# Optimization experiments

Measured on AMD Instinct MI355X. Metric: run time of the kernel, lower is better.

Reference implementation:

```python
import jax, jax.numpy as jnp
import numpy as np

N_NODES = 100000
N_EDGES = 1600000
NFEAT, NHID, NCLASS = 512, 128, 40


def setup_inputs() -> dict:
    key = jax.random.key(0)
    ks = jax.random.split(key, 8)
    x = jax.random.normal(ks[0], (N_NODES, NFEAT), dtype=jnp.float32)
    adj_row = jax.random.randint(ks[1], (N_EDGES,), 0, N_NODES, dtype=jnp.int64)
    adj_col = jax.random.randint(ks[2], (N_EDGES,), 0, N_NODES, dtype=jnp.int64)
    adj_val = jax.random.uniform(ks[3], (N_EDGES,), dtype=jnp.float32)
    W1 = jax.random.normal(ks[4], (NFEAT, NHID), dtype=jnp.float32) * (1.0 / np.sqrt(NHID))
    b1 = jax.random.normal(ks[5], (NHID,), dtype=jnp.float32) * 0.01
    W2 = jax.random.normal(ks[6], (NHID, NCLASS), dtype=jnp.float32) * (1.0 / np.sqrt(NCLASS))
    b2 = jax.random.normal(ks[7], (NCLASS,), dtype=jnp.float32) * 0.01
    return {"x": x, "adj_row": adj_row, "adj_col": adj_col, "adj_val": adj_val,
            "W1": W1, "b1": b1, "W2": W2, "b2": b2}


def _spmm(row, col, val, dense):
    # COO SpMM: out[r] = sum_e val[e] * dense[col[e]]  for edges with row[e]==r
    gathered = val[:, None] * dense[col]          # [E, F]
    return jax.ops.segment_sum(gathered, row, num_segments=N_NODES)


def reference(x, adj_row, adj_col, adj_val, W1, b1, W2, b2):
    # Layer 1: support = X @ W1; out = A @ support + b1; ReLU
    h = _spmm(adj_row, adj_col, adj_val, x @ W1) + b1
    h = jax.nn.relu(h)
    # dropout is identity in eval mode (training=False)
    # Layer 2
    logits = _spmm(adj_row, adj_col, adj_val, h @ W2) + b2
    return jax.nn.log_softmax(logits, axis=1)
```

## Files before the change

kernel.cpp:

```cpp
#include <hip/hip_runtime.h>
#include <hip/hip_bf16.h>
#include <math.h>

#define N_NODES 100000
#define N_EDGES 1600000
#define NFEAT 512
#define NHID 128
#define NCLASS 40
#define GEMM1_BLOCKS ((N_NODES + 255) / 256)
#define COUNT_BLOCKS ((N_EDGES + 255) / 256)
#define CPAD 16

typedef __attribute__((ext_vector_type(8))) short short8;
typedef __attribute__((ext_vector_type(4))) float floatx4;

__device__ __forceinline__ short f2bf(float f) {
    union { float f; unsigned u; } v; v.f = f;
    unsigned r = v.u + 0x7FFFu + ((v.u >> 16) & 1u);
    return (short)(r >> 16);
}
__device__ __forceinline__ float bf2f(unsigned short u) {
    union { unsigned u; float f; } v; v.u = ((unsigned)u) << 16;
    return v.f;
}
__device__ __forceinline__ unsigned pk2bf(float a, float b) {
    __hip_bfloat162 t = __float22bfloat162_rn(make_float2(a, b));
    union { __hip_bfloat162 h; unsigned u; } v; v.h = t;
    return v.u;
}

__global__ void convert_W1_kernel(const float* __restrict__ W1, unsigned short* __restrict__ W1T) {
    int i = blockIdx.x * 256 + threadIdx.x;
    int k = i >> 7, n = i & 127;
    W1T[(size_t)n * NFEAT + k] = (unsigned short)f2bf(W1[i]);
}

__global__ __launch_bounds__(256, 2)
void fusedA_kernel(const float* __restrict__ x, const unsigned short* __restrict__ W1T,
                   unsigned short* __restrict__ out,
                   const int* __restrict__ adj_row, int* __restrict__ countsPad) {
    if (blockIdx.x >= GEMM1_BLOCKS) {
        int e = (blockIdx.x - GEMM1_BLOCKS) * 256 + threadIdx.x;
        if (e < N_EDGES) atomicAdd(&countsPad[(size_t)adj_row[e] * CPAD], 1);
        return;
    }
    int t = threadIdx.x;
    int w = t >> 6, l = t & 63;
    int lane16 = l & 15, quad = l >> 4;
    int rowBase = blockIdx.x * 256 + w * 64;

    floatx4 acc[4][8];
    #pragma unroll
    for (int i = 0; i < 4; i++)
        #pragma unroll
        for (int j = 0; j < 8; j++) acc[i][j] = (floatx4){0.f, 0.f, 0.f, 0.f};

    for (int kc = 0; kc < NFEAT; kc += 32) {
        short8 bfr[8];
        #pragma unroll
        for (int nt = 0; nt < 8; nt++) {
            const unsigned short* bp =
                W1T + (size_t)(nt * 16 + lane16) * NFEAT + kc + quad * 8;
            bfr[nt] = *(const short8*)bp;
        }
        short8 afr[4];
        #pragma unroll
        for (int mt = 0; mt < 4; mt++) {
            int gr = rowBase + mt * 16 + lane16;
            if (gr >= N_NODES) gr = N_NODES - 1;
            const float* ap = x + (size_t)gr * NFEAT + kc + quad * 8;
            float4 v0 = *(const float4*)ap;
            float4 v1 = *(const float4*)(ap + 4);
            union { short8 s; unsigned u[4]; } av;
            av.u[0] = pk2bf(v0.x, v0.y);
            av.u[1] = pk2bf(v0.z, v0.w);
            av.u[2] = pk2bf(v1.x, v1.y);
            av.u[3] = pk2bf(v1.z, v1.w);
            afr[mt] = av.s;
        }
        #pragma unroll
        for (int mt = 0; mt < 4; mt++)
            #pragma unroll
            for (int nt = 0; nt < 8; nt++)
                acc[mt][nt] = __builtin_amdgcn_mfma_f32_16x16x32_bf16(
                    afr[mt], bfr[nt], acc[mt][nt], 0, 0, 0);
    }
    #pragma unroll
    for (int mt = 0; mt < 4; mt++) {
        #pragma unroll
        for (int r = 0; r < 4; r++) {
            int gr = rowBase + mt * 16 + quad * 4 + r;
            if (gr < N_NODES) {
                #pragma unroll
                for (int nt = 0; nt < 8; nt++)
                    out[(size_t)gr * NHID + nt * 16 + lane16] =
                        (unsigned short)f2bf(acc[mt][nt][r]);
            }
        }
    }
}

__global__ void scan1_kernel(const int* __restrict__ countsPad, int* __restrict__ offsets,
                             int* __restrict__ blockSums, int n) {
    __shared__ int sdata[256];
    int t = threadIdx.x;
    int base = blockIdx.x * 1024 + t * 4;
    int v0 = (base + 0 < n) ? countsPad[(size_t)(base + 0) * CPAD] : 0;
    int v1 = (base + 1 < n) ? countsPad[(size_t)(base + 1) * CPAD] : 0;
    int v2 = (base + 2 < n) ? countsPad[(size_t)(base + 2) * CPAD] : 0;
    int v3 = (base + 3 < n) ? countsPad[(size_t)(base + 3) * CPAD] : 0;
    int tot = v0 + v1 + v2 + v3;
    sdata[t] = tot;
    __syncthreads();
    for (int ofs = 1; ofs < 256; ofs <<= 1) {
        int w = (t >= ofs) ? sdata[t - ofs] : 0;
        __syncthreads();
        sdata[t] += w;
        __syncthreads();
    }
    int excl = sdata[t] - tot;
    if (base + 0 < n) offsets[base + 0] = excl;
    if (base + 1 < n) offsets[base + 1] = excl + v0;
    if (base + 2 < n) offsets[base + 2] = excl + v0 + v1;
    if (base + 3 < n) offsets[base + 3] = excl + v0 + v1 + v2;
    if (t == 255) blockSums[blockIdx.x] = sdata[255];
}

__global__ void scan2_kernel(int* __restrict__ blockSums, int nb) {
    __shared__ int sdata[128];
    int t = threadIdx.x;
    int v = (t < nb) ? blockSums[t] : 0;
    sdata[t] = v;
    __syncthreads();
    for (int ofs = 1; ofs < 128; ofs <<= 1) {
        int w = (t >= ofs) ? sdata[t - ofs] : 0;
        __syncthreads();
        sdata[t] += w;
        __syncthreads();
    }
    if (t < nb) blockSums[t] = sdata[t] - v;
}

__global__ void scan3_kernel(int* __restrict__ offsets, const int* __restrict__ blockSums,
                             int* __restrict__ cursorPad, int n, int total) {
    int t = threadIdx.x;
    int base = blockIdx.x * 1024 + t * 4;
    int add = blockSums[blockIdx.x];
    #pragma unroll
    for (int j = 0; j < 4; j++)
        if (base + j < n) {
            int v = offsets[base + j] + add;
            offsets[base + j] = v;
            cursorPad[(size_t)(base + j) * CPAD] = v;
        }
    if (blockIdx.x == 0 && t == 0) offsets[n] = total;
}

__global__ void fill_kernel(const int* __restrict__ row, const int* __restrict__ col,
                            const float* __restrict__ val, int* __restrict__ cursorPad,
                            int2* __restrict__ csr, int E) {
    int e = blockIdx.x * blockDim.x + threadIdx.x;
    if (e < E) {
        int r = row[e];
        int p = atomicAdd(&cursorPad[(size_t)r * CPAD], 1);
        csr[p] = make_int2(col[e], __float_as_int(val[e]));
    }
}

__global__ __launch_bounds__(256)
void spmm1_kernel(const int* __restrict__ offsets, const int2* __restrict__ csr,
                  const unsigned short* __restrict__ dense, const float* __restrict__ b1,
                  unsigned short* __restrict__ h) {
    int r = blockIdx.x * 4 + (threadIdx.x >> 6);
    int l = threadIdx.x & 63;
    int beg = offsets[r], end = offsets[r + 1];
    float acc0 = 0.f, acc1 = 0.f;
    for (int c0 = beg; c0 < end; c0 += 64) {
        int cnt = min(64, end - c0);
        int2 pk = (l < cnt) ? csr[c0 + l] : make_int2(0, 0);
        int j = 0;
        for (; j + 4 <= cnt; j += 4) {
            int cA = __shfl(pk.x, j + 0), cB = __shfl(pk.x, j + 1);
            int cC = __shfl(pk.x, j + 2), cD = __shfl(pk.x, j + 3);
            float vA = __int_as_float(__shfl(pk.y, j + 0));
            float vB = __int_as_float(__shfl(pk.y, j + 1));
            float vC = __int_as_float(__shfl(pk.y, j + 2));
            float vD = __int_as_float(__shfl(pk.y, j + 3));
            unsigned dA = *(const unsigned*)&dense[(size_t)cA * NHID + l * 2];
            unsigned dB = *(const unsigned*)&dense[(size_t)cB * NHID + l * 2];
            unsigned dC = *(const unsigned*)&dense[(size_t)cC * NHID + l * 2];
            unsigned dD = *(const unsigned*)&dense[(size_t)cD * NHID + l * 2];
            acc0 += vA * bf2f((unsigned short)dA) + vB * bf2f((unsigned short)dB)
                  + vC * bf2f((unsigned short)dC) + vD * bf2f((unsigned short)dD);
            acc1 += vA * bf2f((unsigned short)(dA >> 16)) + vB * bf2f((unsigned short)(dB >> 16))
                  + vC * bf2f((unsigned short)(dC >> 16)) + vD * bf2f((unsigned short)(dD >> 16));
        }
        for (; j < cnt; j++) {
            int c = __shfl(pk.x, j);
            float v = __int_as_float(__shfl(pk.y, j));
            unsigned d = *(const unsigned*)&dense[(size_t)c * NHID + l * 2];
            acc0 += v * bf2f((unsigned short)d);
            acc1 += v * bf2f((unsigned short)(d >> 16));
        }
    }
    float r0 = fmaxf(acc0 + b1[l * 2 + 0], 0.f);
    float r1 = fmaxf(acc1 + b1[l * 2 + 1], 0.f);
    unsigned packed = ((unsigned)(unsigned short)f2bf(r0)) |
                      (((unsigned)(unsigned short)f2bf(r1)) << 16);
    *(unsigned*)&h[(size_t)r * NHID + l * 2] = packed;
}

__global__ __launch_bounds__(256)
void gemm2_kernel(const unsigned short* __restrict__ h, const float* __restrict__ W2,
                  unsigned short* __restrict__ out) {
    __shared__ float W2s[NHID * NCLASS];
    __shared__ float hs[4][NHID];
    int t = threadIdx.x;
    for (int i = t; i < NHID * NCLASS; i += 256) W2s[i] = W2[i];
    int row0 = blockIdx.x * 4;
    int rr = t >> 6, l = t & 63;
    {
        unsigned d = *(const unsigned*)&h[(size_t)(row0 + rr) * NHID + l * 2];
        hs[rr][l * 2 + 0] = bf2f((unsigned short)d);
        hs[rr][l * 2 + 1] = bf2f((unsigned short)(d >> 16));
    }
    __syncthreads();
    if (l < NCLASS) {
        float acc = 0.f;
        #pragma unroll 8
        for (int k = 0; k < NHID; k++) acc += hs[rr][k] * W2s[k * NCLASS + l];
        out[(size_t)(row0 + rr) * NCLASS + l] = (unsigned short)f2bf(acc);
    }
}

__global__ __launch_bounds__(256)
void spmm2_kernel(const int* __restrict__ offsets, const int2* __restrict__ csr,
                  const unsigned short* __restrict__ dense, const float* __restrict__ b2,
                  float* __restrict__ out) {
    int r = blockIdx.x * 4 + (threadIdx.x >> 6);
    int l = threadIdx.x & 63;
    int beg = offsets[r], end = offsets[r + 1];
    float acc = 0.f;
    for (int c0 = beg; c0 < end; c0 += 64) {
        int cnt = min(64, end - c0);
        int2 pk = (l < cnt) ? csr[c0 + l] : make_int2(0, 0);
        int j = 0;
        for (; j + 4 <= cnt; j += 4) {
            int cA = __shfl(pk.x, j + 0), cB = __shfl(pk.x, j + 1);
            int cC = __shfl(pk.x, j + 2), cD = __shfl(pk.x, j + 3);
            float vA = __int_as_float(__shfl(pk.y, j + 0));
            float vB = __int_as_float(__shfl(pk.y, j + 1));
            float vC = __int_as_float(__shfl(pk.y, j + 2));
            float vD = __int_as_float(__shfl(pk.y, j + 3));
            if (l < NCLASS) {
                float fA = bf2f(dense[(size_t)cA * NCLASS + l]);
                float fB = bf2f(dense[(size_t)cB * NCLASS + l]);
                float fC = bf2f(dense[(size_t)cC * NCLASS + l]);
                float fD = bf2f(dense[(size_t)cD * NCLASS + l]);
                acc += vA * fA + vB * fB + vC * fC + vD * fD;
            }
        }
        for (; j < cnt; j++) {
            int c = __shfl(pk.x, j);
            float v = __int_as_float(__shfl(pk.y, j));
            if (l < NCLASS) acc += v * bf2f(dense[(size_t)c * NCLASS + l]);
        }
    }
    float logit = (l < NCLASS) ? (acc + b2[l]) : -INFINITY;
    float m = logit;
    #pragma unroll
    for (int o = 32; o >= 1; o >>= 1) m = fmaxf(m, __shfl_xor(m, o, 64));
    float e = (l < NCLASS) ? __expf(logit - m) : 0.f;
    float s = e;
    #pragma unroll
    for (int o = 32; o >= 1; o >>= 1) s += __shfl_xor(s, o, 64);
    if (l < NCLASS) out[(size_t)r * NCLASS + l] = logit - m - __logf(s);
}


extern "C" void kernel_launch(void* const* d_in, const int* in_sizes, int n_in,
                              void* d_out, int out_size, void* d_ws, size_t ws_size,
                              hipStream_t stream) {
    const float* x       = (const float*)d_in[0];
    const int*   adj_row = (const int*)d_in[1];
    const int*   adj_col = (const int*)d_in[2];
    const float* adj_val = (const float*)d_in[3];
    const float* W1      = (const float*)d_in[4];
    const float* b1      = (const float*)d_in[5];
    const float* W2      = (const float*)d_in[6];
    const float* b2      = (const float*)d_in[7];
    float* out = (float*)d_out;

    char* ws = (char*)d_ws;
    size_t off = 0;
    auto alloc = [&](size_t bytes) -> void* {
        void* p = ws + off;
        off += bytes;
        off = (off + 255) & ~(size_t)255;
        return p;
    };
    unsigned short* support1 = (unsigned short*)alloc((size_t)N_NODES * NHID * 2);
    unsigned short* h        = (unsigned short*)alloc((size_t)N_NODES * NHID * 2);
    unsigned short* support2 = (unsigned short*)alloc((size_t)N_NODES * NCLASS * 2);
    unsigned short* W1T      = (unsigned short*)alloc((size_t)NFEAT * NHID * 2);
    int*   offsets   = (int*)alloc((size_t)(N_NODES + 4) * 4);
    int*   countsPad = (int*)alloc((size_t)N_NODES * CPAD * 4);
    int*   blockSums = (int*)alloc(1024 * 4);
    int2*  csr       = (int2*)alloc((size_t)N_EDGES * 8);

    hipMemsetAsync(countsPad, 0, (size_t)N_NODES * CPAD * sizeof(int), stream);
    convert_W1_kernel<<<(NFEAT * NHID) / 256, 256, 0, stream>>>(W1, W1T);
    fusedA_kernel<<<GEMM1_BLOCKS + COUNT_BLOCKS, 256, 0, stream>>>(
        x, W1T, support1, adj_row, countsPad);
    int nblk = (N_NODES + 1023) / 1024;
    scan1_kernel<<<nblk, 256, 0, stream>>>(countsPad, offsets, blockSums, N_NODES);
    scan2_kernel<<<1, 128, 0, stream>>>(blockSums, nblk);
    scan3_kernel<<<nblk, 256, 0, stream>>>(offsets, blockSums, countsPad, N_NODES, N_EDGES);
    fill_kernel<<<COUNT_BLOCKS, 256, 0, stream>>>(adj_row, adj_col, adj_val,
                                                  countsPad, csr, N_EDGES);
    spmm1_kernel<<<N_NODES / 4, 256, 0, stream>>>(offsets, csr, support1, b1, h);
    gemm2_kernel<<<N_NODES / 4, 256, 0, stream>>>(h, W2, support2);
    spmm2_kernel<<<N_NODES / 4, 256, 0, stream>>>(offsets, csr, support2, b2, out);
}
```

Baseline: 689.3 us.

## Record edge ranks during counting, shrink GEMM1 tiles, batch GEMM2 rows, unroll SpMM gathers

Result: no change. 682.8 us (-0.9%).

```diff
diff --git a/kernel.cpp b/kernel.cpp
--- a/kernel.cpp
+++ b/kernel.cpp
@@ -7,8 +7,8 @@
 #define NFEAT 512
 #define NHID 128
 #define NCLASS 40
-#define GEMM1_BLOCKS ((N_NODES + 255) / 256)
-#define COUNT_BLOCKS ((N_EDGES + 255) / 256)
+#define GEMM1_BLOCKS ((N_NODES + 63) / 64)
+#define COUNT_BLOCKS ((N_EDGES + 1023) / 1024)
 #define CPAD 16
 
 typedef __attribute__((ext_vector_type(8))) short short8;
@@ -35,67 +35,62 @@
     W1T[(size_t)n * NFEAT + k] = (unsigned short)f2bf(W1[i]);
 }
 
-__global__ __launch_bounds__(256, 2)
+__global__ __launch_bounds__(256)
 void fusedA_kernel(const float* __restrict__ x, const unsigned short* __restrict__ W1T,
                    unsigned short* __restrict__ out,
-                   const int* __restrict__ adj_row, int* __restrict__ countsPad) {
+                   const int* __restrict__ adj_row, int* __restrict__ countsPad,
+                   unsigned short* __restrict__ ranks) {
     if (blockIdx.x >= GEMM1_BLOCKS) {
-        int e = (blockIdx.x - GEMM1_BLOCKS) * 256 + threadIdx.x;
-        if (e < N_EDGES) atomicAdd(&countsPad[(size_t)adj_row[e] * CPAD], 1);
+        int base = (blockIdx.x - GEMM1_BLOCKS) * 1024 + threadIdx.x;
+        int e0 = base, e1 = base + 256, e2 = base + 512, e3 = base + 768;
+        int r0 = (e0 < N_EDGES) ? adj_row[e0] : -1;
+        int r1 = (e1 < N_EDGES) ? adj_row[e1] : -1;
+        int r2 = (e2 < N_EDGES) ? adj_row[e2] : -1;
+        int r3 = (e3 < N_EDGES) ? adj_row[e3] : -1;
+        if (r0 >= 0) ranks[e0] = (unsigned short)atomicAdd(&countsPad[(size_t)r0 * CPAD], 1);
+        if (r1 >= 0) ranks[e1] = (unsigned short)atomicAdd(&countsPad[(size_t)r1 * CPAD], 1);
+        if (r2 >= 0) ranks[e2] = (unsigned short)atomicAdd(&countsPad[(size_t)r2 * CPAD], 1);
+        if (r3 >= 0) ranks[e3] = (unsigned short)atomicAdd(&countsPad[(size_t)r3 * CPAD], 1);
         return;
     }
     int t = threadIdx.x;
     int w = t >> 6, l = t & 63;
     int lane16 = l & 15, quad = l >> 4;
-    int rowBase = blockIdx.x * 256 + w * 64;
-
-    floatx4 acc[4][8];
-    #pragma unroll
-    for (int i = 0; i < 4; i++)
-        #pragma unroll
-        for (int j = 0; j < 8; j++) acc[i][j] = (floatx4){0.f, 0.f, 0.f, 0.f};
+    int rowBase = blockIdx.x * 64 + w * 16;
+
+    floatx4 acc[8];
+    #pragma unroll
+    for (int j = 0; j < 8; j++) acc[j] = (floatx4){0.f, 0.f, 0.f, 0.f};
+
+    int gr = rowBase + lane16;
+    if (gr >= N_NODES) gr = N_NODES - 1;
+    const float* aRow = x + (size_t)gr * NFEAT + quad * 8;
 
     for (int kc = 0; kc < NFEAT; kc += 32) {
-        short8 bfr[8];
+        float4 v0 = *(const float4*)(aRow + kc);
+        float4 v1 = *(const float4*)(aRow + kc + 4);
+        union { short8 s; unsigned u[4]; } av;
+        av.u[0] = pk2bf(v0.x, v0.y);
+        av.u[1] = pk2bf(v0.z, v0.w);
+        av.u[2] = pk2bf(v1.x, v1.y);
+        av.u[3] = pk2bf(v1.z, v1.w);
+        short8 afr = av.s;
         #pragma unroll
         for (int nt = 0; nt < 8; nt++) {
             const unsigned short* bp =
                 W1T + (size_t)(nt * 16 + lane16) * NFEAT + kc + quad * 8;
-            bfr[nt] = *(const short8*)bp;
-        }
-        short8 afr[4];
-        #pragma unroll
-        for (int mt = 0; mt < 4; mt++) {
-            int gr = rowBase + mt * 16 + lane16;
-            if (gr >= N_NODES) gr = N_NODES - 1;
-            const float* ap = x + (size_t)gr * NFEAT + kc + quad * 8;
-            float4 v0 = *(const float4*)ap;
-            float4 v1 = *(const float4*)(ap + 4);
-            union { short8 s; unsigned u[4]; } av;
-            av.u[0] = pk2bf(v0.x, v0.y);
-            av.u[1] = pk2bf(v0.z, v0.w);
-            av.u[2] = pk2bf(v1.x, v1.y);
-            av.u[3] = pk2bf(v1.z, v1.w);
-            afr[mt] = av.s;
-        }
-        #pragma unroll
-        for (int mt = 0; mt < 4; mt++)
+            short8 bfr = *(const short8*)bp;
+            acc[nt] = __builtin_amdgcn_mfma_f32_16x16x32_bf16(afr, bfr, acc[nt], 0, 0, 0);
+        }
+    }
+    #pragma unroll
+    for (int r = 0; r < 4; r++) {
+        int gr2 = rowBase + quad * 4 + r;
+        if (gr2 < N_NODES) {
             #pragma unroll
             for (int nt = 0; nt < 8; nt++)
-                acc[mt][nt] = __builtin_amdgcn_mfma_f32_16x16x32_bf16(
-                    afr[mt], bfr[nt], acc[mt][nt], 0, 0, 0);
-    }
-    #pragma unroll
-    for (int mt = 0; mt < 4; mt++) {
-        #pragma unroll
-        for (int r = 0; r < 4; r++) {
-            int gr = rowBase + mt * 16 + quad * 4 + r;
-            if (gr < N_NODES) {
-                #pragma unroll
-                for (int nt = 0; nt < 8; nt++)
-                    out[(size_t)gr * NHID + nt * 16 + lane16] =
-                        (unsigned short)f2bf(acc[mt][nt][r]);
-            }
+                out[(size_t)gr2 * NHID + nt * 16 + lane16] =
+                    (unsigned short)f2bf(acc[nt][r]);
         }
     }
 }
@@ -142,28 +137,29 @@
 }
 
 __global__ void scan3_kernel(int* __restrict__ offsets, const int* __restrict__ blockSums,
-                             int* __restrict__ cursorPad, int n, int total) {
+                             int n, int total) {
     int t = threadIdx.x;
     int base = blockIdx.x * 1024 + t * 4;
     int add = blockSums[blockIdx.x];
     #pragma unroll
     for (int j = 0; j < 4; j++)
-        if (base + j < n) {
-            int v = offsets[base + j] + add;
-            offsets[base + j] = v;
-            cursorPad[(size_t)(base + j) * CPAD] = v;
-        }
+        if (base + j < n) offsets[base + j] += add;
     if (blockIdx.x == 0 && t == 0) offsets[n] = total;
 }
 
-__global__ void fill_kernel(const int* __restrict__ row, const int* __restrict__ col,
-                            const float* __restrict__ val, int* __restrict__ cursorPad,
-                            int2* __restrict__ csr, int E) {
-    int e = blockIdx.x * blockDim.x + threadIdx.x;
-    if (e < E) {
-        int r = row[e];
-        int p = atomicAdd(&cursorPad[(size_t)r * CPAD], 1);
-        csr[p] = make_int2(col[e], __float_as_int(val[e]));
+__global__ __launch_bounds__(256)
+void fill_kernel(const int* __restrict__ row, const int* __restrict__ col,
+                 const float* __restrict__ val, const int* __restrict__ offsets,
+                 const unsigned short* __restrict__ ranks, int2* __restrict__ csr) {
+    int base = blockIdx.x * 1024 + threadIdx.x;
+    #pragma unroll
+    for (int i = 0; i < 4; i++) {
+        int e = base + i * 256;
+        if (e < N_EDGES) {
+            int r = row[e];
+            int p = offsets[r] + (int)ranks[e];
+            csr[p] = make_int2(col[e], __float_as_int(val[e]));
+        }
     }
 }
 
@@ -179,21 +175,20 @@
         int cnt = min(64, end - c0);
         int2 pk = (l < cnt) ? csr[c0 + l] : make_int2(0, 0);
         int j = 0;
-        for (; j + 4 <= cnt; j += 4) {
-            int cA = __shfl(pk.x, j + 0), cB = __shfl(pk.x, j + 1);
-            int cC = __shfl(pk.x, j + 2), cD = __shfl(pk.x, j + 3);
-            float vA = __int_as_float(__shfl(pk.y, j + 0));
-            float vB = __int_as_float(__shfl(pk.y, j + 1));
-            float vC = __int_as_float(__shfl(pk.y, j + 2));
-            float vD = __int_as_float(__shfl(pk.y, j + 3));
-            unsigned dA = *(const unsigned*)&dense[(size_t)cA * NHID + l * 2];
-            unsigned dB = *(const unsigned*)&dense[(size_t)cB * NHID + l * 2];
-            unsigned dC = *(const unsigned*)&dense[(size_t)cC * NHID + l * 2];
-            unsigned dD = *(const unsigned*)&dense[(size_t)cD * NHID + l * 2];
-            acc0 += vA * bf2f((unsigned short)dA) + vB * bf2f((unsigned short)dB)
-                  + vC * bf2f((unsigned short)dC) + vD * bf2f((unsigned short)dD);
-            acc1 += vA * bf2f((unsigned short)(dA >> 16)) + vB * bf2f((unsigned short)(dB >> 16))
-                  + vC * bf2f((unsigned short)(dC >> 16)) + vD * bf2f((unsigned short)(dD >> 16));
+        for (; j + 8 <= cnt; j += 8) {
+            unsigned d[8];
+            float v[8];
+            #pragma unroll
+            for (int q = 0; q < 8; q++) {
+                int c = __shfl(pk.x, j + q);
+                v[q] = __int_as_float(__shfl(pk.y, j + q));
+                d[q] = *(const unsigned*)&dense[(size_t)c * NHID + l * 2];
+            }
+            #pragma unroll
+            for (int q = 0; q < 8; q++) {
+                acc0 += v[q] * bf2f((unsigned short)d[q]);
+                acc1 += v[q] * bf2f((unsigned short)(d[q] >> 16));
+            }
         }
         for (; j < cnt; j++) {
             int c = __shfl(pk.x, j);
@@ -205,31 +200,42 @@
     }
     float r0 = fmaxf(acc0 + b1[l * 2 + 0], 0.f);
     float r1 = fmaxf(acc1 + b1[l * 2 + 1], 0.f);
-    unsigned packed = ((unsigned)(unsigned short)f2bf(r0)) |
-                      (((unsigned)(unsigned short)f2bf(r1)) << 16);
-    *(unsigned*)&h[(size_t)r * NHID + l * 2] = packed;
+    *(unsigned*)&h[(size_t)r * NHID + l * 2] = pk2bf(r0, r1);
 }
 
 __global__ __launch_bounds__(256)
 void gemm2_kernel(const unsigned short* __restrict__ h, const float* __restrict__ W2,
                   unsigned short* __restrict__ out) {
     __shared__ float W2s[NHID * NCLASS];
-    __shared__ float hs[4][NHID];
+    __shared__ float hs[32][NHID];
     int t = threadIdx.x;
     for (int i = t; i < NHID * NCLASS; i += 256) W2s[i] = W2[i];
-    int row0 = blockIdx.x * 4;
-    int rr = t >> 6, l = t & 63;
+    int row0 = blockIdx.x * 32;
     {
-        unsigned d = *(const unsigned*)&h[(size_t)(row0 + rr) * NHID + l * 2];
-        hs[rr][l * 2 + 0] = bf2f((unsigned short)d);
-        hs[rr][l * 2 + 1] = bf2f((unsigned short)(d >> 16));
+        const unsigned* hsrc = (const unsigned*)(h + (size_t)row0 * NHID);
+        #pragma unroll
+        for (int j = 0; j < 8; j++) {
+            int f = t * 8 + j;
+            unsigned d = hsrc[f];
+            hs[f >> 6][(f & 63) * 2 + 0] = bf2f((unsigned short)d);
+            hs[f >> 6][(f & 63) * 2 + 1] = bf2f((unsigned short)(d >> 16));
+        }
     }
     __syncthreads();
+    int w = t >> 6, l = t & 63;
     if (l < NCLASS) {
-        float acc = 0.f;
-        #pragma unroll 8
-        for (int k = 0; k < NHID; k++) acc += hs[rr][k] * W2s[k * NCLASS + l];
-        out[(size_t)(row0 + rr) * NCLASS + l] = (unsigned short)f2bf(acc);
+        float acc[8];
+        #pragma unroll
+        for (int j = 0; j < 8; j++) acc[j] = 0.f;
+        #pragma unroll 4
+        for (int k = 0; k < NHID; k++) {
+            float wk = W2s[k * NCLASS + l];
+            #pragma unroll
+            for (int j = 0; j < 8; j++) acc[j] += hs[w * 8 + j][k] * wk;
+        }
+        #pragma unroll
+        for (int j = 0; j < 8; j++)
+            out[(size_t)(row0 + w * 8 + j) * NCLASS + l] = (unsigned short)f2bf(acc[j]);
     }
 }
 
@@ -245,20 +251,16 @@
         int cnt = min(64, end - c0);
         int2 pk = (l < cnt) ? csr[c0 + l] : make_int2(0, 0);
         int j = 0;
-        for (; j + 4 <= cnt; j += 4) {
-            int cA = __shfl(pk.x, j + 0), cB = __shfl(pk.x, j + 1);
-            int cC = __shfl(pk.x, j + 2), cD = __shfl(pk.x, j + 3);
-            float vA = __int_as_float(__shfl(pk.y, j + 0));
-            float vB = __int_as_float(__shfl(pk.y, j + 1));
-            float vC = __int_as_float(__shfl(pk.y, j + 2));
-            float vD = __int_as_float(__shfl(pk.y, j + 3));
-            if (l < NCLASS) {
-                float fA = bf2f(dense[(size_t)cA * NCLASS + l]);
-                float fB = bf2f(dense[(size_t)cB * NCLASS + l]);
-                float fC = bf2f(dense[(size_t)cC * NCLASS + l]);
-                float fD = bf2f(dense[(size_t)cD * NCLASS + l]);
-                acc += vA * fA + vB * fB + vC * fC + vD * fD;
+        for (; j + 8 <= cnt; j += 8) {
+            float v[8], f[8];
+            #pragma unroll
+            for (int q = 0; q < 8; q++) {
+                int c = __shfl(pk.x, j + q);
+                v[q] = __int_as_float(__shfl(pk.y, j + q));
+                f[q] = (l < NCLASS) ? bf2f(dense[(size_t)c * NCLASS + l]) : 0.f;
             }
+            #pragma unroll
+            for (int q = 0; q < 8; q++) acc += v[q] * f[q];
         }
         for (; j < cnt; j++) {
             int c = __shfl(pk.x, j);
@@ -306,19 +308,20 @@
     int*   offsets   = (int*)alloc((size_t)(N_NODES + 4) * 4);
     int*   countsPad = (int*)alloc((size_t)N_NODES * CPAD * 4);
     int*   blockSums = (int*)alloc(1024 * 4);
+    unsigned short* ranks = (unsigned short*)alloc((size_t)N_EDGES * 2);
     int2*  csr       = (int2*)alloc((size_t)N_EDGES * 8);
 
     hipMemsetAsync(countsPad, 0, (size_t)N_NODES * CPAD * sizeof(int), stream);
     convert_W1_kernel<<<(NFEAT * NHID) / 256, 256, 0, stream>>>(W1, W1T);
     fusedA_kernel<<<GEMM1_BLOCKS + COUNT_BLOCKS, 256, 0, stream>>>(
-        x, W1T, support1, adj_row, countsPad);
+        x, W1T, support1, adj_row, countsPad, ranks);
     int nblk = (N_NODES + 1023) / 1024;
     scan1_kernel<<<nblk, 256, 0, stream>>>(countsPad, offsets, blockSums, N_NODES);
     scan2_kernel<<<1, 128, 0, stream>>>(blockSums, nblk);
-    scan3_kernel<<<nblk, 256, 0, stream>>>(offsets, blockSums, countsPad, N_NODES, N_EDGES);
+    scan3_kernel<<<nblk, 256, 0, stream>>>(offsets, blockSums, N_NODES, N_EDGES);
     fill_kernel<<<COUNT_BLOCKS, 256, 0, stream>>>(adj_row, adj_col, adj_val,
-                                                  countsPad, csr, N_EDGES);
+                                                  offsets, ranks, csr);
     spmm1_kernel<<<N_NODES / 4, 256, 0, stream>>>(offsets, csr, support1, b1, h);
-    gemm2_kernel<<<N_NODES / 4, 256, 0, stream>>>(h, W2, support2);
+    gemm2_kernel<<<N_NODES / 32, 256, 0, stream>>>(h, W2, support2);
     spmm2_kernel<<<N_NODES / 4, 256, 0, stream>>>(offsets, csr, support2, b2, out);
 }
```
